# Performance work log

Hardware: AMD Instinct MI355X
Metric: run time of the kernel (lower is better)

## Reference

```python
import jax, jax.numpy as jnp
import numpy as np

THETA = 1.0  # integrate-and-fire threshold


def conv2d_t(x, w, b, padding):
    # x: [N,C,H,W,T]; torch snn.conv is Conv3d with kernel (k,k,1) => per-timestep 2D conv
    N, C, H, W, T = x.shape
    xt = jnp.moveaxis(x, -1, 1).reshape(N * T, C, H, W)
    y = jax.lax.conv_general_dilated(
        xt, w, (1, 1), [(padding, padding), (padding, padding)],
        dimension_numbers=('NCHW', 'OIHW', 'NCHW'))
    y = y + b[None, :, None, None]
    O, Ho, Wo = y.shape[1:]
    return jnp.moveaxis(y.reshape(N, T, O, Ho, Wo), 1, -1)


def avg_pool2_t(x):
    # snn.pool(2): fixed-weight 2x2 conv == 2x2 average pool, applied per timestep
    N, C, H, W, T = x.shape
    return x.reshape(N, C, H // 2, 2, W // 2, 2, T).mean(axis=(3, 5))


def dense_t(x, w, b):
    # snn.dense: Conv3d over full spatial extent == linear over flattened C*H*W, per timestep
    N = x.shape[0]; T = x.shape[-1]
    xf = x.reshape(N, -1, T)  # flatten in (C,H,W) order, matching torch conv3d weight layout
    return jnp.einsum('nft,of->not', xf, w) + b[None, :, None]


def spike(x):
    # Temporal LIF (integrate-and-fire, soft reset) scanned over trailing time dim.
    def step(u, xt):
        u = u + xt
        s = (u >= THETA).astype(x.dtype)
        u = u - s * THETA
        return u, s
    xt = jnp.moveaxis(x, -1, 0)  # [T, ...]
    _, s = jax.lax.scan(step, jnp.zeros(x.shape[:-1], x.dtype), xt)
    return jnp.moveaxis(s, 0, -1)


def setup_inputs() -> dict:
    key = jax.random.key(0)
    ks = jax.random.split(key, 20)
    f32 = jnp.float32
    def w(k, shape, fan_in):
        return jax.random.normal(k, shape, f32) * np.float32(1.0 / np.sqrt(fan_in))
    inp = {
        'x':  jax.random.uniform(ks[0], (128, 1, 28, 28, 16), f32),
        'w1': w(ks[1], (32, 1, 3, 3), 9),      'b1': jnp.zeros((32,), f32),
        'w2': w(ks[2], (32, 32, 3, 3), 288),   'b2': jnp.zeros((32,), f32),
        'w3': w(ks[3], (32, 32, 3, 3), 288),   'b3': jnp.zeros((32,), f32),
        'w4': w(ks[4], (16, 32, 1, 1), 32),    'b4': jnp.zeros((16,), f32),
        'w5': w(ks[5], (16, 16, 3, 3), 144),   'b5': jnp.zeros((16,), f32),
        'w6': w(ks[6], (32, 16, 1, 1), 16),    'b6': jnp.zeros((32,), f32),
        'wf1': w(ks[7], (128, 32 * 14 * 14), 32 * 14 * 14), 'bf1': jnp.zeros((128,), f32),
        'wf2': w(ks[8], (10, 128), 128),       'bf2': jnp.zeros((10,), f32),
    }
    return inp


def reference(x, w1, b1, w2, b2, w3, b3, w4, b4, w5, b5, w6, b6, wf1, bf1, wf2, bf2):
    T = x.shape[-1]
    h = spike(conv2d_t(x, w1, b1, 1))
    y = h
    h = spike(conv2d_t(h, w2, b2, 1))
    h = spike(conv2d_t(h, w3, b3, 1) + y)
    h = spike(avg_pool2_t(h))
    y1 = h
    h = spike(conv2d_t(h, w4, b4, 0))
    h = spike(conv2d_t(h, w5, b5, 1))
    h = spike(conv2d_t(h, w6, b6, 0) + y1)
    h = spike(dense_t(h, wf1, bf1))
    h = spike(dense_t(h, wf2, bf2))
    return h.sum(axis=-1) / T  # [N, 10] firing rates
```

## Files before the change

kernel.cpp:

```cpp
#include <hip/hip_runtime.h>

typedef unsigned short u16;
typedef unsigned int u32;
typedef unsigned long long u64;
typedef __attribute__((ext_vector_type(4))) int i32x4;
typedef __attribute__((ext_vector_type(16))) int i32x16;

#define TT 16
#define Z16 {0, 0, 0, 0, 0, 0, 0, 0, 0, 0, 0, 0, 0, 0, 0, 0}

__device__ __forceinline__ u32 scan_spike(const double* acc) {
  double u = 0.0;
  u32 m = 0;
#pragma unroll
  for (int t = 0; t < TT; ++t) {
    u += acc[t];
    if (u >= 1.0) { m |= (1u << t); u -= 1.0; }
  }
  return m;
}

__device__ __forceinline__ long long shfl_xor64(long long v, int m) {
  int lo = __shfl_xor((int)(v & 0xffffffffLL), m);
  int hi = __shfl_xor((int)(v >> 32), m);
  return ((long long)hi << 32) | (u32)lo;
}

__device__ __forceinline__ float conv1_fetch(const float* __restrict__ xn,
                                             int y0, int r, int col, int t) {
  int yi = y0 - 1 + r, xi = col - 1;
  if ((unsigned)yi < 28u && (unsigned)xi < 28u)
    return xn[((size_t)(yi * 28 + xi)) * 16 + t];
  return 0.0f;
}

__global__ __launch_bounds__(448) void conv1_lds(
    const float* __restrict__ x, const float* __restrict__ w,
    const float* __restrict__ b, u16* __restrict__ out) {
  __shared__ float xt[2][4][30][20];
  __shared__ float wl[32][9];

  int blk = blockIdx.x;
  int n = blk >> 1;
  int half = blk & 1;
  int ypBase = half * 7;
  int tid = threadIdx.x;

  for (int i = tid; i < 288; i += 448) wl[i / 9][i % 9] = w[i];

  int sr_[5], sc_[5], st_[5];
  bool sok[5];
#pragma unroll
  for (int k = 0; k < 5; ++k) {
    int i = tid + k * 448;
    sok[k] = (i < 1920);
    int ii = sok[k] ? i : 0;
    sr_[k] = ii / 480;
    int rem = ii % 480;
    sc_[k] = rem / 16;
    st_[k] = rem % 16;
  }
  const float* xn = x + (size_t)n * (28 * 28 * 16);

  int ocg = tid & 7;
  int xx = (tid >> 3) % 28;
  int dy = tid / 224;
  int oc0 = ocg * 4;

  {
    int y0 = ypBase * 2;
#pragma unroll
    for (int k = 0; k < 5; ++k)
      if (sok[k])
        xt[0][sr_[k]][sc_[k]][st_[k]] =
            conv1_fetch(xn, y0, sr_[k], sc_[k], st_[k]);
  }
  __syncthreads();

  float wr[4][9];
#pragma unroll
  for (int j = 0; j < 4; ++j)
#pragma unroll
    for (int ko = 0; ko < 9; ++ko) wr[j][ko] = wl[oc0 + j][ko];
  float bf[4];
#pragma unroll
  for (int j = 0; j < 4; ++j) bf[j] = b[oc0 + j];

  for (int it = 0; it < 7; ++it) {
    int y0 = (ypBase + it) * 2;
    int cur = it & 1;

    float pf[5];
    if (it < 6) {
      int y0n = y0 + 2;
#pragma unroll
      for (int k = 0; k < 5; ++k)
        pf[k] = sok[k] ? conv1_fetch(xn, y0n, sr_[k], sc_[k], st_[k]) : 0.0f;
    }

    double u[4] = {0.0, 0.0, 0.0, 0.0};
    u32 m[4] = {0u, 0u, 0u, 0u};

    const float* row0 = &xt[cur][dy + 0][xx][0];
    const float* row1 = &xt[cur][dy + 1][xx][0];
    const float* row2 = &xt[cur][dy + 2][xx][0];

#pragma unroll
    for (int q = 0; q < 4; ++q) {
      float4 xq[9];
#pragma unroll
      for (int kx = 0; kx < 3; ++kx) {
        xq[0 * 3 + kx] = *(const float4*)(row0 + kx * 20 + q * 4);
        xq[1 * 3 + kx] = *(const float4*)(row1 + kx * 20 + q * 4);
        xq[2 * 3 + kx] = *(const float4*)(row2 + kx * 20 + q * 4);
      }
#pragma unroll
      for (int j = 0; j < 4; ++j) {
        float4 s = {0.0f, 0.0f, 0.0f, 0.0f};
#pragma unroll
        for (int ko = 0; ko < 9; ++ko) {
          s.x = fmaf(wr[j][ko], xq[ko].x, s.x);
          s.y = fmaf(wr[j][ko], xq[ko].y, s.y);
          s.z = fmaf(wr[j][ko], xq[ko].z, s.z);
          s.w = fmaf(wr[j][ko], xq[ko].w, s.w);
        }
        float y0f = s.x + bf[j], y1f = s.y + bf[j];
        float y2f = s.z + bf[j], y3f = s.w + bf[j];
        u[j] += (double)y0f;
        if (u[j] >= 1.0) { m[j] |= 1u << (4 * q + 0); u[j] -= 1.0; }
        u[j] += (double)y1f;
        if (u[j] >= 1.0) { m[j] |= 1u << (4 * q + 1); u[j] -= 1.0; }
        u[j] += (double)y2f;
        if (u[j] >= 1.0) { m[j] |= 1u << (4 * q + 2); u[j] -= 1.0; }
        u[j] += (double)y3f;
        if (u[j] >= 1.0) { m[j] |= 1u << (4 * q + 3); u[j] -= 1.0; }
      }
    }

    int yo = y0 + dy;
    u64 pk = (u64)(u16)m[0] | ((u64)(u16)m[1] << 16) |
             ((u64)(u16)m[2] << 32) | ((u64)(u16)m[3] << 48);
    *(u64*)(out + ((size_t)(n * 28 + yo) * 28 + xx) * 32 + oc0) = pk;

    if (it < 6) {
      int nb = (it + 1) & 1;
#pragma unroll
      for (int k = 0; k < 5; ++k)
        if (sok[k]) xt[nb][sr_[k]][sc_[k]][st_[k]] = pf[k];
      __syncthreads();
    }
  }
}

__global__ void prep_digits_frag2(const float* __restrict__ wa,
                                  const float* __restrict__ wb,
                                  signed char* __restrict__ Wda,
                                  signed char* __restrict__ Wdb) {
  int bid = blockIdx.x;
  const float* w = (bid < 9) ? wa : wb;
  signed char* Wd = (bid < 9) ? Wda : Wdb;
  int tap = bid % 9;
  int lane = threadIdx.x;
  int oc = lane & 31, kh = lane >> 5;
  for (int j = 0; j < 16; ++j) {
    int c = kh * 16 + j;
    double xv = ldexp((double)w[((size_t)(oc * 32 + c)) * 9 + tap], 29);
    long long X = (long long)rint(xv);
    for (int p = 0; p < 4; ++p) {
      int d = (int)((X + 128) & 255) - 128;
      Wd[((size_t)((p * 9 + tap) * 64 + lane)) * 16 + j] = (signed char)d;
      X = (X - (long long)d) >> 8;
    }
  }
}

__global__ void prep_digits5c(const float* __restrict__ w,
                              signed char* __restrict__ Wd) {
  int tap = blockIdx.x;
  int lane = threadIdx.x;
  int oc = lane & 31, kh = lane >> 5;
  for (int j = 0; j < 16; ++j) {
    long long X = 0;
    if (oc < 16 && kh == 0) {
      double xv = ldexp((double)w[((size_t)(oc * 16 + j)) * 9 + tap], 29);
      X = (long long)rint(xv);
    }
    for (int p = 0; p < 4; ++p) {
      int d = (int)((X + 128) & 255) - 128;
      Wd[((size_t)((p * 9 + tap) * 64 + lane)) * 16 + j] = (signed char)d;
      X = (X - (long long)d) >> 8;
    }
  }
}

__global__ __launch_bounds__(256) void zero_borders(
    signed char* __restrict__ T1, signed char* __restrict__ T2) {
  const int PER = 128 * 116 * 32;
  int idx = blockIdx.x * 256 + threadIdx.x;
  int buf = idx >= PER;
  int r = buf ? idx - PER : idx;
  if (r >= PER) return;
  int c16 = r & 31;
  int site = (r >> 5) % 116;
  int nloc = (r >> 5) / 116;
  int y, x;
  if (site < 30) { y = 0; x = site; }
  else if (site < 60) { y = 29; x = site - 30; }
  else if (site < 88) { x = 0; y = site - 60 + 1; }
  else { x = 29; y = site - 88 + 1; }
  signed char* T = buf ? T2 : T1;
  *(i32x4*)(T + (((size_t)nloc * 30 + y) * 30 + x) * 512 + c16 * 16) =
      (i32x4){0, 0, 0, 0};
}

__global__ __launch_bounds__(256) void expand_masks(
    const u16* __restrict__ s, signed char* __restrict__ T) {
  int site = blockIdx.x * 8 + (threadIdx.x >> 5);
  int gl = threadIdx.x & 31;
  int x = site % 28; int t1 = site / 28;
  int y = t1 % 28;   int nloc = t1 / 28;

  u32 v = (u32)s[(((size_t)nloc * 28 + y) * 28 + x) * 32 + gl];
  const u32 MK[5] = {0x0000FFFFu, 0x00FF00FFu, 0x0F0F0F0Fu,
                     0x33333333u, 0x55555555u};
#pragma unroll
  for (int i = 0; i < 5; ++i) {
    int sh = 16 >> i;
    u32 mk = MK[i];
    u32 p = (u32)__shfl_xor((int)v, sh);
    v = ((gl & sh) == 0) ? ((v & mk) | ((p & mk) << sh))
                         : ((v & ~mk) | ((p & ~mk) >> sh));
  }
  if (gl < 16) {
    u32 dw[8];
#pragma unroll
    for (int d = 0; d < 8; ++d) {
      u32 nib = (v >> (4 * d)) & 0xFu;
      dw[d] = (nib * 0x00204081u) & 0x01010101u;
    }
    signed char* Tp =
        T + (((size_t)nloc * 30 + y + 1) * 30 + (x + 1)) * 512 + gl * 32;
    *(i32x4*)Tp = (i32x4){(int)dw[0], (int)dw[1], (int)dw[2], (int)dw[3]};
    *(i32x4*)(Tp + 16) = (i32x4){(int)dw[4], (int)dw[5], (int)dw[6], (int)dw[7]};
  }
}

__global__ __launch_bounds__(256) void expand_t5c(
    const u16* __restrict__ s, signed char* __restrict__ T) {
  int site = blockIdx.x * 8 + (threadIdx.x >> 5);
  int gl = threadIdx.x & 31;
  int x = site % 14; int t1 = site / 14;
  int y = t1 % 14;   int n = t1 / 14;

  u32 v = 0;
  if (gl < 16) v = (u32)s[(((size_t)n * 16 + gl) * 14 + y) * 14 + x];
  const u32 MK[5] = {0x0000FFFFu, 0x00FF00FFu, 0x0F0F0F0Fu,
                     0x33333333u, 0x55555555u};
#pragma unroll
  for (int i = 0; i < 5; ++i) {
    int sh = 16 >> i;
    u32 mk = MK[i];
    u32 p = (u32)__shfl_xor((int)v, sh);
    v = ((gl & sh) == 0) ? ((v & mk) | ((p & mk) << sh))
                         : ((v & ~mk) | ((p & ~mk) >> sh));
  }
  if (gl < 16) {
    u32 dw[4];
#pragma unroll
    for (int d = 0; d < 4; ++d) {
      u32 nib = (v >> (4 * d)) & 0xFu;
      dw[d] = (nib * 0x00204081u) & 0x01010101u;
    }
    signed char* Tp =
        T + ((((size_t)n * 16 + y + 1) * 16 + (x + 1))) * 512 + gl * 32;
    *(i32x4*)Tp = (i32x4){(int)dw[0], (int)dw[1], (int)dw[2], (int)dw[3]};
    *(i32x4*)(Tp + 16) = (i32x4){0, 0, 0, 0};
  }
}

template <int H, int W, int PADW, int COUT, bool WRITE_T, bool HAS_RES>
__device__ __forceinline__ void epi_i8(long long (&cc)[16], int h, int oc,
                                       int px_out, int y, int nloc, int n_g,
                                       const float* bias,
                                       const u16* __restrict__ res,
                                       signed char* __restrict__ Tout,
                                       u16* __restrict__ mout) {
  long long recv[8];
#pragma unroll
  for (int j = 0; j < 8; ++j) {
    long long send = h ? cc[j] : cc[8 + j];
    recv[j] = shfl_xor64(send, 32);
  }
  long long B29 = 0;
  if (oc < COUT) B29 = (long long)rint((double)bias[oc] * 536870912.0);
  u32 rm = 0;
  if (HAS_RES && px_out < W)
    rm = res[(((size_t)n_g * H + y) * W + px_out) * COUT + oc];
  long long u = 0;
  u32 mo = 0;
  const long long TH = 1LL << 29;
#pragma unroll
  for (int t = 0; t < TT; ++t) {
    int lo = (t & 3) + 4 * (t >> 3);
    int sel = (t >> 2) & 1;
    long long own = h ? cc[8 + lo] : cc[lo];
    long long ut = (sel ^ h) ? recv[lo] : own;
    ut += B29 + (((rm >> t) & 1u) ? TH : 0);
    u += ut;
    if (u >= TH) { mo |= (1u << t); u -= TH; }
  }
  if (px_out < W && oc < COUT) {
    if (WRITE_T) {
      signed char* Tp =
          Tout + (((size_t)nloc * PADW + y + 1) * PADW + px_out + 1) * 512 + oc;
#pragma unroll
      for (int t = 0; t < TT; ++t)
        Tp[t * 32] = (signed char)((mo >> t) & 1u);
    } else {
      mout[(((size_t)n_g * COUT + oc) * H + y) * W + px_out] = (u16)mo;
    }
  }
}

template <int H, int W, int PADW, int COUT, bool WRITE_T, bool HAS_RES>
__global__ __launch_bounds__(256, 2) void conv_i8(
    const signed char* __restrict__ Tin, const signed char* __restrict__ Wd,
    const float* __restrict__ bias, const u16* __restrict__ res,
    signed char* __restrict__ Tout, u16* __restrict__ mout, int nbase) {
  constexpr int TILESX = (W + 15) / 16;
  __shared__ signed char WL[4 * 9 * 1024];
  int tid = threadIdx.x;
  for (int j = tid; j < 2304; j += 256)
    ((i32x4*)WL)[j] = ((const i32x4*)Wd)[j];
  __syncthreads();

  int blk = blockIdx.x;
  int xblk = blk % TILESX; int b2 = blk / TILESX;
  int y = b2 % H;          int nloc = b2 / H;
  int lane = tid & 63, wid = tid >> 6;
  int h = lane >> 5, rowlane = lane & 31;
  int pxr = rowlane >> 4, tA = rowlane & 15;
  int pxb = xblk * 16 + wid * 4;

  i32x4 A0[9], A1[9];
  const signed char* Tn = Tin + (size_t)nloc * (PADW * PADW * 512);
#pragma unroll
  for (int ky = 0; ky < 3; ++ky)
#pragma unroll
    for (int kx = 0; kx < 3; ++kx) {
      int tap = ky * 3 + kx;
      int ypad = y + ky;
      int x0 = pxb + pxr + kx;     if (x0 > PADW - 1) x0 = PADW - 1;
      int x1 = pxb + 2 + pxr + kx; if (x1 > PADW - 1) x1 = PADW - 1;
      A0[tap] = *(const i32x4*)(Tn + ((size_t)(ypad * PADW + x0)) * 512 +
                                tA * 32 + h * 16);
      A1[tap] = *(const i32x4*)(Tn + ((size_t)(ypad * PADW + x1)) * 512 +
                                tA * 32 + h * 16);
    }

  i32x16 cp0[2], cp1[2];
#pragma unroll
  for (int pp = 0; pp < 2; ++pp) {
    i32x16 a0lo = Z16, a0hi = Z16, a1lo = Z16, a1hi = Z16;
#pragma unroll
    for (int tap = 0; tap < 9; ++tap) {
      i32x4 Blo =
          *(const i32x4*)&WL[((size_t)(((2 * pp) * 9 + tap) * 64 + lane)) * 16];
      i32x4 Bhi = *(const i32x4*)&WL[((size_t)(((2 * pp + 1) * 9 + tap) * 64 +
                                               lane)) * 16];
      a0lo = __builtin_amdgcn_mfma_i32_32x32x32_i8(A0[tap], Blo, a0lo, 0, 0, 0);
      a0hi = __builtin_amdgcn_mfma_i32_32x32x32_i8(A0[tap], Bhi, a0hi, 0, 0, 0);
      a1lo = __builtin_amdgcn_mfma_i32_32x32x32_i8(A1[tap], Blo, a1lo, 0, 0, 0);
      a1hi = __builtin_amdgcn_mfma_i32_32x32x32_i8(A1[tap], Bhi, a1hi, 0, 0, 0);
    }
#pragma unroll
    for (int r = 0; r < 16; ++r) {
      cp0[pp][r] = a0lo[r] + (a0hi[r] << 8);
      cp1[pp][r] = a1lo[r] + (a1hi[r] << 8);
    }
  }

  long long c0[16], c1[16];
#pragma unroll
  for (int r = 0; r < 16; ++r) {
    c0[r] = (long long)cp0[0][r] + ((long long)cp0[1][r] << 16);
    c1[r] = (long long)cp1[0][r] + ((long long)cp1[1][r] << 16);
  }

  int n_g = nbase + nloc;
  int oc = rowlane;
  epi_i8<H, W, PADW, COUT, WRITE_T, HAS_RES>(c0, h, oc, pxb + h, y, nloc, n_g,
                                             bias, res, Tout, mout);
  epi_i8<H, W, PADW, COUT, WRITE_T, HAS_RES>(c1, h, oc, pxb + 2 + h, y, nloc,
                                             n_g, bias, res, Tout, mout);
}

__global__ __launch_bounds__(256) void pool_spike(
    const u16* __restrict__ in, u16* __restrict__ out) {
  int idx = blockIdx.x * 256 + threadIdx.x;
  const int total = 128 * 32 * 14 * 14;
  if (idx >= total) return;
  int xx = idx % 14; int t1 = idx / 14;
  int yy = t1 % 14;  int t2 = t1 / 14;
  int c  = t2 % 32;  int n  = t2 / 32;

  const u16* base = in + ((size_t)(n * 32 + c) * 28 + yy * 2) * 28 + xx * 2;
  u32 m00 = base[0], m01 = base[1], m10 = base[28], m11 = base[29];

  double acc[TT];
#pragma unroll
  for (int t = 0; t < TT; ++t) {
    u32 s = ((m00 >> t) & 1u) + ((m01 >> t) & 1u) + ((m10 >> t) & 1u) +
            ((m11 >> t) & 1u);
    acc[t] = 0.25 * (double)s;
  }
  out[idx] = (u16)scan_spike(acc);
}

template <int CIN>
__global__ __launch_bounds__(256) void conv1x1_spike(
    const u16* __restrict__ in, const float* __restrict__ w,
    const float* __restrict__ b, const u16* __restrict__ res,
    u16* __restrict__ out, int N, int Cout, int HW) {
  int idx = blockIdx.x * 256 + threadIdx.x;
  int total = N * Cout * HW;
  if (idx >= total) return;
  int p = idx % HW; int t1 = idx / HW;
  int o = t1 % Cout; int n = t1 / Cout;

  double acc[TT];
  double bv = (double)b[o];
#pragma unroll
  for (int t = 0; t < TT; ++t) acc[t] = bv;

  const u16* inp = in + (size_t)n * CIN * HW + p;
  const float* wo = w + (size_t)o * CIN;
#pragma unroll 4
  for (int c = 0; c < CIN; ++c) {
    u32 m = inp[c * HW];
    double wh = 0.5 * (double)wo[c];
#pragma unroll
    for (int t = 0; t < TT; ++t) {
      u32 hi = (m << (30 - t)) & 0x40000000u;
      acc[t] = fma(wh, __hiloint2double((int)hi, 0), acc[t]);
    }
  }
  if (res) {
    u32 m = res[idx];
#pragma unroll
    for (int t = 0; t < TT; ++t) acc[t] += ((m >> t) & 1u) ? 1.0 : 0.0;
  }
  out[idx] = (u16)scan_spike(acc);
}

__global__ __launch_bounds__(256) void expand_t7(
    const u16* __restrict__ s, signed char* __restrict__ T) {
  int site = blockIdx.x * 8 + (threadIdx.x >> 5);
  int gl = threadIdx.x & 31;
  int fc = site % 196; int n = site / 196;

  u32 v = (u32)s[(size_t)n * 6272 + fc * 32 + gl];
  const u32 MK[5] = {0x0000FFFFu, 0x00FF00FFu, 0x0F0F0F0Fu,
                     0x33333333u, 0x55555555u};
#pragma unroll
  for (int i = 0; i < 5; ++i) {
    int sh = 16 >> i;
    u32 mk = MK[i];
    u32 p = (u32)__shfl_xor((int)v, sh);
    v = ((gl & sh) == 0) ? ((v & mk) | ((p & mk) << sh))
                         : ((v & ~mk) | ((p & ~mk) >> sh));
  }
  if (gl < 16) {
    u32 dw[8];
#pragma unroll
    for (int d = 0; d < 8; ++d) {
      u32 nib = (v >> (4 * d)) & 0xFu;
      dw[d] = (nib * 0x00204081u) & 0x01010101u;
    }
    signed char* Tp = T + ((size_t)n * 16 + gl) * 6272 + fc * 32;
    *(i32x4*)Tp = (i32x4){(int)dw[0], (int)dw[1], (int)dw[2], (int)dw[3]};
    *(i32x4*)(Tp + 16) = (i32x4){(int)dw[4], (int)dw[5], (int)dw[6], (int)dw[7]};
  }
}

__global__ __launch_bounds__(256) void prep_dense_digits(
    const float* __restrict__ w, signed char* __restrict__ Wd) {
  int linear = blockIdx.x * 256 + threadIdx.x;
  int lane = linear & 63;
  int kc = (linear >> 6) % 196;
  int pg = (linear >> 6) / 196;
  int p = pg % 6, g = pg / 6;
  int col = lane & 31, kh = lane >> 5;
  int o = g * 32 + col, fb = kc * 32 + kh * 16;

  alignas(16) signed char dig[16];
#pragma unroll
  for (int j = 0; j < 16; ++j) {
    double xv = (double)w[(size_t)o * 6272 + fb + j] * 35184372088832.0;
    long long X = (long long)rint(xv);
    unsigned long long Y = (unsigned long long)(X + 0x808080808080LL);
    dig[j] = (signed char)(int)(((Y >> (8 * p)) & 255u) - 128);
  }
  *(i32x4*)(Wd + (size_t)linear * 16) = *(const i32x4*)dig;
}

__global__ __launch_bounds__(256) void dense1_part(
    const signed char* __restrict__ T7, const signed char* __restrict__ Wd,
    long long* __restrict__ Pbuf) {
  __shared__ long long red[3][64][16];
  int tid = threadIdx.x, lane = tid & 63, wid = tid >> 6;
  int bidx = blockIdx.x;
  int Mt = bidx & 63;
  int g = (bidx >> 6) & 3;
  int ks = bidx >> 8;
  int n0 = Mt * 2;
  int nl = (lane >> 4) & 1, tA = lane & 15, kh = lane >> 5;

  const signed char* Arow =
      T7 + ((size_t)(n0 + nl) * 16 + tA) * 6272 + kh * 16;
  const signed char* Bbase = Wd + (size_t)g * 6 * 196 * 1024 + lane * 16;

  int slot = ks * 4 + wid;
  int kc0 = slot * 12 + (slot < 4 ? slot : 4);
  int len = (slot < 4) ? 13 : 12;

  i32x16 acc[6];
#pragma unroll
  for (int p = 0; p < 6; ++p)
#pragma unroll
    for (int r = 0; r < 16; ++r) acc[p][r] = 0;

  for (int kc = kc0; kc < kc0 + len; ++kc) {
    i32x4 Af = *(const i32x4*)(Arow + (size_t)kc * 32);
#pragma unroll
    for (int p = 0; p < 6; ++p) {
      i32x4 Bf = *(const i32x4*)(Bbase + (size_t)(p * 196 + kc) * 1024);
      acc[p] = __builtin_amdgcn_mfma_i32_32x32x32_i8(Af, Bf, acc[p], 0, 0, 0);
    }
  }

  long long cc[16];
#pragma unroll
  for (int r = 0; r < 16; ++r) {
    long long v = 0;
#pragma unroll
    for (int p = 0; p < 6; ++p) v += ((long long)acc[p][r]) << (8 * p);
    cc[r] = v;
  }

  if (wid) {
#pragma unroll
    for (int r = 0; r < 16; ++r) red[wid - 1][lane][r] = cc[r];
  }
  __syncthreads();
  if (wid == 0) {
#pragma unroll
    for (int w2 = 0; w2 < 3; ++w2)
#pragma unroll
      for (int r = 0; r < 16; ++r) cc[r] += red[w2][lane][r];
    long long* P = Pbuf + ((size_t)(ks * 256 + Mt * 4 + g)) * 1024 + lane * 16;
#pragma unroll
    for (int r = 0; r < 16; ++r) P[r] = cc[r];
  }
}

__global__ __launch_bounds__(64) void dense1_scan(
    const long long* __restrict__ Pbuf, const float* __restrict__ bias,
    u16* __restrict__ out) {
  int bidx = blockIdx.x;
  int lane = threadIdx.x;
  int g = bidx & 3, n0 = (bidx >> 2) * 2;

  long long cc[16];
#pragma unroll
  for (int r = 0; r < 16; ++r) cc[r] = 0;
#pragma unroll
  for (int ks = 0; ks < 4; ++ks) {
    const long long* P =
        Pbuf + ((size_t)(ks * 256 + bidx)) * 1024 + lane * 16;
#pragma unroll
    for (int r = 0; r < 16; ++r) cc[r] += P[r];
  }

  int h = lane >> 5, col = lane & 31;
  long long recv[8];
#pragma unroll
  for (int j = 0; j < 8; ++j) {
    long long send = h ? cc[j] : cc[8 + j];
    recv[j] = shfl_xor64(send, 32);
  }
  long long B45 =
      (long long)rint((double)bias[g * 32 + col] * 35184372088832.0);
  long long u = 0;
  u32 mo = 0;
  const long long TH = 1LL << 45;
#pragma unroll
  for (int t = 0; t < TT; ++t) {
    int lo = (t & 3) + 4 * (t >> 3);
    int sel = (t >> 2) & 1;
    long long own = h ? cc[8 + lo] : cc[lo];
    long long ut = (sel ^ h) ? recv[lo] : own;
    ut += B45;
    u += ut;
    if (u >= TH) { mo |= (1u << t); u -= TH; }
  }
  out[(n0 + h) * 128 + g * 32 + col] = (u16)mo;
}

__global__ __launch_bounds__(64) void dense2_out(
    const u16* __restrict__ in, const float* __restrict__ w,
    const float* __restrict__ b, float* __restrict__ out) {
  int idx = blockIdx.x * 64 + threadIdx.x;
  if (idx >= 1280) return;
  int o = idx % 10;
  int n = idx / 10;

  double acc[TT];
  double bv = (double)b[o];
#pragma unroll
  for (int t = 0; t < TT; ++t) acc[t] = bv;

  const u16* inn = in + (size_t)n * 128;
  const float* wo = w + (size_t)o * 128;
  for (int f = 0; f < 128; ++f) {
    u32 m = inn[f];
    double wv = (double)wo[f];
#pragma unroll
    for (int t = 0; t < TT; ++t) acc[t] += ((m >> t) & 1u) ? wv : 0.0;
  }
  u32 mo = scan_spike(acc);
  out[idx] = (float)__popc(mo) * 0.0625f;
}

extern "C" void kernel_launch(void* const* d_in, const int* in_sizes, int n_in,
                              void* d_out, int out_size, void* d_ws,
                              size_t ws_size, hipStream_t stream) {
  const float* x   = (const float*)d_in[0];
  const float* w1  = (const float*)d_in[1];
  const float* b1  = (const float*)d_in[2];
  const float* w2  = (const float*)d_in[3];
  const float* b2  = (const float*)d_in[4];
  const float* w3  = (const float*)d_in[5];
  const float* b3  = (const float*)d_in[6];
  const float* w4  = (const float*)d_in[7];
  const float* b4  = (const float*)d_in[8];
  const float* w5  = (const float*)d_in[9];
  const float* b5  = (const float*)d_in[10];
  const float* w6  = (const float*)d_in[11];
  const float* b6  = (const float*)d_in[12];
  const float* wf1 = (const float*)d_in[13];
  const float* bf1 = (const float*)d_in[14];
  const float* wf2 = (const float*)d_in[15];
  const float* bf2 = (const float*)d_in[16];
  float* out = (float*)d_out;

  char* W = (char*)d_ws;
  u16* s1 = (u16*)(W + 0);
  u16* s3 = (u16*)(W + 6422528);
  u16* s4 = (u16*)(W + 12845056);
  u16* s5 = (u16*)(W + 14450688);
  u16* s6 = (u16*)(W + 15253504);
  u16* s7 = (u16*)(W + 16056320);
  u16* s8 = (u16*)(W + 17661952);
  signed char* Wd2 = (signed char*)(W + 17694720);
  signed char* Wd3 = (signed char*)(W + 17750016);
  signed char* T1f = (signed char*)(W + 17805312);
  signed char* T2f = (signed char*)(W + 76787712);
  signed char* T5c  = T1f;
  signed char* Wd5c = (signed char*)(W + 34582528);
  signed char* Wd1 = T2f;
  long long*  Pbuf = (long long*)((char*)T2f + 5242880);
  signed char* T7  = T1f;

  prep_digits_frag2<<<18, 64, 0, stream>>>(w2, w3, Wd2, Wd3);
  zero_borders<<<3712, 256, 0, stream>>>(T1f, T2f);

  conv1_lds<<<256, 448, 0, stream>>>(x, w1, b1, s1);

  expand_masks<<<12544, 256, 0, stream>>>(s1, T1f);
  conv_i8<28, 28, 30, 32, true, false><<<7168, 256, 0, stream>>>(
      T1f, Wd2, b2, nullptr, T2f, nullptr, 0);
  conv_i8<28, 28, 30, 32, false, true><<<7168, 256, 0, stream>>>(
      T2f, Wd3, b3, s1, nullptr, s3, 0);

  pool_spike<<<3136, 256, 0, stream>>>(s3, s4);
  conv1x1_spike<32><<<1568, 256, 0, stream>>>(s4, w4, b4, nullptr, s5, 128, 16,
                                              196);
  hipMemsetAsync(T5c, 0, 16777216, stream);
  prep_digits5c<<<9, 64, 0, stream>>>(w5, Wd5c);
  expand_t5c<<<3136, 256, 0, stream>>>(s5, T5c);
  conv_i8<14, 14, 16, 16, false, false><<<1792, 256, 0, stream>>>(
      T5c, Wd5c, b5, nullptr, nullptr, s6, 0);
  conv1x1_spike<16><<<3136, 256, 0, stream>>>(s6, w6, b6, s4, s7, 128, 32, 196);

  expand_t7<<<3136, 256, 0, stream>>>(s7, T7);
  prep_dense_digits<<<1176, 256, 0, stream>>>(wf1, Wd1);
  dense1_part<<<1024, 256, 0, stream>>>(T7, Wd1, Pbuf);
  dense1_scan<<<256, 64, 0, stream>>>(Pbuf, bf1, s8);

  dense2_out<<<20, 64, 0, stream>>>(s8, wf2, bf2, out);
}
```

Measured before the change: 512.3 us.

## Make int8 conv blocks persistent and prefetch next tile's A fragments

The int8 MFMA conv kernel now processes several tiles per block (14 for the 28x28 convs, 4 for the 14x14 conv) instead of one tile per block. This amortizes the per-block LDS weight load and sync across many tiles. The A-operand loads for the next tile are issued after the MFMAs and before the epilogue, so global loads can overlap epilogue work. The cost is more register pressure from live prefetched fragments, fewer blocks for latency hiding, and a serial per-block loop. The nbase argument is dropped, and n_g is replaced by nloc.

```diff
diff --git a/kernel.cpp b/kernel.cpp
--- a/kernel.cpp
+++ b/kernel.cpp
@@ -322,11 +322,12 @@
   }
 }
 
-template <int H, int W, int PADW, int COUT, bool WRITE_T, bool HAS_RES>
+template <int H, int W, int PADW, int COUT, bool WRITE_T, bool HAS_RES,
+          int IPB>
 __global__ __launch_bounds__(256, 2) void conv_i8(
     const signed char* __restrict__ Tin, const signed char* __restrict__ Wd,
     const float* __restrict__ bias, const u16* __restrict__ res,
-    signed char* __restrict__ Tout, u16* __restrict__ mout, int nbase) {
+    signed char* __restrict__ Tout, u16* __restrict__ mout, int total) {
   constexpr int TILESX = (W + 15) / 16;
   __shared__ signed char WL[4 * 9 * 1024];
   int tid = threadIdx.x;
@@ -334,65 +335,85 @@
     ((i32x4*)WL)[j] = ((const i32x4*)Wd)[j];
   __syncthreads();
 
-  int blk = blockIdx.x;
-  int xblk = blk % TILESX; int b2 = blk / TILESX;
-  int y = b2 % H;          int nloc = b2 / H;
   int lane = tid & 63, wid = tid >> 6;
   int h = lane >> 5, rowlane = lane & 31;
   int pxr = rowlane >> 4, tA = rowlane & 15;
-  int pxb = xblk * 16 + wid * 4;
+  int laneoff = tA * 32 + h * 16;
+
+  int base = blockIdx.x * IPB;
+  int cnt = total - base;
+  if (cnt > IPB) cnt = IPB;
+  if (cnt <= 0) return;
 
   i32x4 A0[9], A1[9];
-  const signed char* Tn = Tin + (size_t)nloc * (PADW * PADW * 512);
-#pragma unroll
-  for (int ky = 0; ky < 3; ++ky)
-#pragma unroll
-    for (int kx = 0; kx < 3; ++kx) {
-      int tap = ky * 3 + kx;
-      int ypad = y + ky;
-      int x0 = pxb + pxr + kx;     if (x0 > PADW - 1) x0 = PADW - 1;
-      int x1 = pxb + 2 + pxr + kx; if (x1 > PADW - 1) x1 = PADW - 1;
-      A0[tap] = *(const i32x4*)(Tn + ((size_t)(ypad * PADW + x0)) * 512 +
-                                tA * 32 + h * 16);
-      A1[tap] = *(const i32x4*)(Tn + ((size_t)(ypad * PADW + x1)) * 512 +
-                                tA * 32 + h * 16);
-    }
-
-  i32x16 cp0[2], cp1[2];
-#pragma unroll
-  for (int pp = 0; pp < 2; ++pp) {
-    i32x16 a0lo = Z16, a0hi = Z16, a1lo = Z16, a1hi = Z16;
-#pragma unroll
-    for (int tap = 0; tap < 9; ++tap) {
-      i32x4 Blo =
-          *(const i32x4*)&WL[((size_t)(((2 * pp) * 9 + tap) * 64 + lane)) * 16];
-      i32x4 Bhi = *(const i32x4*)&WL[((size_t)(((2 * pp + 1) * 9 + tap) * 64 +
-                                               lane)) * 16];
-      a0lo = __builtin_amdgcn_mfma_i32_32x32x32_i8(A0[tap], Blo, a0lo, 0, 0, 0);
-      a0hi = __builtin_amdgcn_mfma_i32_32x32x32_i8(A0[tap], Bhi, a0hi, 0, 0, 0);
-      a1lo = __builtin_amdgcn_mfma_i32_32x32x32_i8(A1[tap], Blo, a1lo, 0, 0, 0);
-      a1hi = __builtin_amdgcn_mfma_i32_32x32x32_i8(A1[tap], Bhi, a1hi, 0, 0, 0);
-    }
+  auto loadA = [&](int item) {
+    int xblk = item % TILESX;
+    int b2 = item / TILESX;
+    int yy = b2 % H;
+    int nl = b2 / H;
+    const signed char* Tn = Tin + (size_t)nl * (PADW * PADW * 512);
+    int pxb = xblk * 16 + wid * 4;
+#pragma unroll
+    for (int ky = 0; ky < 3; ++ky)
+#pragma unroll
+      for (int kx = 0; kx < 3; ++kx) {
+        int tap = ky * 3 + kx;
+        int ypad = yy + ky;
+        int x0 = pxb + pxr + kx;     if (x0 > PADW - 1) x0 = PADW - 1;
+        int x1 = pxb + 2 + pxr + kx; if (x1 > PADW - 1) x1 = PADW - 1;
+        A0[tap] = *(const i32x4*)(Tn + ((size_t)(ypad * PADW + x0)) * 512 +
+                                  laneoff);
+        A1[tap] = *(const i32x4*)(Tn + ((size_t)(ypad * PADW + x1)) * 512 +
+                                  laneoff);
+      }
+  };
+
+  loadA(base);
+  for (int k = 0; k < cnt; ++k) {
+    int item = base + k;
+    int xblk = item % TILESX;
+    int b2 = item / TILESX;
+    int y = b2 % H;
+    int nloc = b2 / H;
+    int pxb = xblk * 16 + wid * 4;
+
+    i32x16 cp0[2], cp1[2];
+#pragma unroll
+    for (int pp = 0; pp < 2; ++pp) {
+      i32x16 a0lo = Z16, a0hi = Z16, a1lo = Z16, a1hi = Z16;
+#pragma unroll
+      for (int tap = 0; tap < 9; ++tap) {
+        i32x4 Blo = *(const i32x4*)&WL[((size_t)(((2 * pp) * 9 + tap) * 64 +
+                                                 lane)) * 16];
+        i32x4 Bhi = *(const i32x4*)&WL[((size_t)(((2 * pp + 1) * 9 + tap) * 64 +
+                                                 lane)) * 16];
+        a0lo = __builtin_amdgcn_mfma_i32_32x32x32_i8(A0[tap], Blo, a0lo, 0, 0, 0);
+        a0hi = __builtin_amdgcn_mfma_i32_32x32x32_i8(A0[tap], Bhi, a0hi, 0, 0, 0);
+        a1lo = __builtin_amdgcn_mfma_i32_32x32x32_i8(A1[tap], Blo, a1lo, 0, 0, 0);
+        a1hi = __builtin_amdgcn_mfma_i32_32x32x32_i8(A1[tap], Bhi, a1hi, 0, 0, 0);
+      }
+#pragma unroll
+      for (int r = 0; r < 16; ++r) {
+        cp0[pp][r] = a0lo[r] + (a0hi[r] << 8);
+        cp1[pp][r] = a1lo[r] + (a1hi[r] << 8);
+      }
+    }
+
+    if (k + 1 < cnt) loadA(item + 1);
+
+    long long c0[16], c1[16];
 #pragma unroll
     for (int r = 0; r < 16; ++r) {
-      cp0[pp][r] = a0lo[r] + (a0hi[r] << 8);
-      cp1[pp][r] = a1lo[r] + (a1hi[r] << 8);
-    }
-  }
-
-  long long c0[16], c1[16];
-#pragma unroll
-  for (int r = 0; r < 16; ++r) {
-    c0[r] = (long long)cp0[0][r] + ((long long)cp0[1][r] << 16);
-    c1[r] = (long long)cp1[0][r] + ((long long)cp1[1][r] << 16);
-  }
-
-  int n_g = nbase + nloc;
-  int oc = rowlane;
-  epi_i8<H, W, PADW, COUT, WRITE_T, HAS_RES>(c0, h, oc, pxb + h, y, nloc, n_g,
-                                             bias, res, Tout, mout);
-  epi_i8<H, W, PADW, COUT, WRITE_T, HAS_RES>(c1, h, oc, pxb + 2 + h, y, nloc,
-                                             n_g, bias, res, Tout, mout);
+      c0[r] = (long long)cp0[0][r] + ((long long)cp0[1][r] << 16);
+      c1[r] = (long long)cp1[0][r] + ((long long)cp1[1][r] << 16);
+    }
+
+    int oc = rowlane;
+    epi_i8<H, W, PADW, COUT, WRITE_T, HAS_RES>(c0, h, oc, pxb + h, y, nloc,
+                                               nloc, bias, res, Tout, mout);
+    epi_i8<H, W, PADW, COUT, WRITE_T, HAS_RES>(c1, h, oc, pxb + 2 + h, y, nloc,
+                                               nloc, bias, res, Tout, mout);
+  }
 }
 
 __global__ __launch_bounds__(256) void pool_spike(
@@ -678,10 +699,10 @@
   conv1_lds<<<256, 448, 0, stream>>>(x, w1, b1, s1);
 
   expand_masks<<<12544, 256, 0, stream>>>(s1, T1f);
-  conv_i8<28, 28, 30, 32, true, false><<<7168, 256, 0, stream>>>(
-      T1f, Wd2, b2, nullptr, T2f, nullptr, 0);
-  conv_i8<28, 28, 30, 32, false, true><<<7168, 256, 0, stream>>>(
-      T2f, Wd3, b3, s1, nullptr, s3, 0);
+  conv_i8<28, 28, 30, 32, true, false, 14><<<512, 256, 0, stream>>>(
+      T1f, Wd2, b2, nullptr, T2f, nullptr, 7168);
+  conv_i8<28, 28, 30, 32, false, true, 14><<<512, 256, 0, stream>>>(
+      T2f, Wd3, b3, s1, nullptr, s3, 7168);
 
   pool_spike<<<3136, 256, 0, stream>>>(s3, s4);
   conv1x1_spike<32><<<1568, 256, 0, stream>>>(s4, w4, b4, nullptr, s5, 128, 16,
@@ -689,8 +710,8 @@
   hipMemsetAsync(T5c, 0, 16777216, stream);
   prep_digits5c<<<9, 64, 0, stream>>>(w5, Wd5c);
   expand_t5c<<<3136, 256, 0, stream>>>(s5, T5c);
-  conv_i8<14, 14, 16, 16, false, false><<<1792, 256, 0, stream>>>(
-      T5c, Wd5c, b5, nullptr, nullptr, s6, 0);
+  conv_i8<14, 14, 16, 16, false, false, 4><<<448, 256, 0, stream>>>(
+      T5c, Wd5c, b5, nullptr, nullptr, s6, 1792);
   conv1x1_spike<16><<<3136, 256, 0, stream>>>(s6, w6, b6, s4, s7, 128, 32, 196);
 
   expand_t7<<<3136, 256, 0, stream>>>(s7, T7);
```

Measured after the change: 663.6 us. 1.3x slower.
